# Performance work log

Measured on AMD Instinct MI355X. Metric: run time of the kernel, lower is better.

Reference implementation:

```python
import jax, jax.numpy as jnp
import numpy as np
import math

FMAPS = [(80, 0.06), (40, 0.12), (20, 0.24), (10, 0.48), (5, 0.72)]
SPLITS = [0, 6400, 8000, 8400, 8500, 8525]
N_LEVELS = 5
N_CAND = 9
ALPHA_REG = 1.0   # config.reg_weights
GAMMA, F_ALPHA = 2.0, 0.25


def _make_priors():
    ps = []
    for f, s in FMAPS:
        c = (np.arange(f, dtype=np.float32) + 0.5) / f
        cy, cx = np.meshgrid(c, c, indexing="ij")
        ps.append(np.stack([cx.ravel(), cy.ravel(),
                            np.full(f * f, s, np.float32),
                            np.full(f * f, s, np.float32)], 1))
    return jnp.asarray(np.concatenate(ps, 0))


def cxcy_to_xy(b):
    return jnp.concatenate([b[..., :2] - b[..., 2:] / 2, b[..., :2] + b[..., 2:] / 2], -1)


def xy_to_cxcy(b):
    return jnp.concatenate([(b[..., :2] + b[..., 2:]) / 2, b[..., 2:] - b[..., :2]], -1)


def gcxgcy_to_cxcy(g, priors):
    cxcy = g[..., :2] * priors[..., 2:] / 10.0 + priors[..., :2]
    wh = jnp.exp(g[..., 2:] / 5.0) * priors[..., 2:]
    return jnp.concatenate([cxcy, wh], -1)


def iou_matrix(a, b):  # a [K,4] corners, b [P,4] corners -> [K,P]
    lt = jnp.maximum(a[:, None, :2], b[None, :, :2])
    rb = jnp.minimum(a[:, None, 2:], b[None, :, 2:])
    wh = jnp.clip(rb - lt, 0.0)
    inter = wh[..., 0] * wh[..., 1]
    area_a = (a[:, 2] - a[:, 0]) * (a[:, 3] - a[:, 1])
    area_b = (b[:, 2] - b[:, 0]) * (b[:, 3] - b[:, 1])
    return inter / (area_a[:, None] + area_b[None, :] - inter)


def _assign_image(boxes_i, labels_i, locs_i, priors):
    # boxes_i [K,4] xyxy, labels_i [K] int, locs_i [P,4] encoded offsets
    gt_cxcy = xy_to_cxcy(boxes_i)
    per_level, pos_ov_all = [], []
    for l in range(N_LEVELS):
        pl = priors[SPLITS[l]:SPLITS[l + 1]]                       # [Pl,4] cxcywh
        dist = jnp.linalg.norm(gt_cxcy[:, None, :2] - pl[None, :, :2], axis=-1)  # [K,Pl]
        _, top_idx = jax.lax.top_k(-dist, N_CAND)                  # [K,9] closest priors
        ov = iou_matrix(boxes_i, cxcy_to_xy(pl))                   # [K,Pl]
        pos_ov = jnp.take_along_axis(ov, top_idx, axis=1)          # [K,9]
        pos_ov_all.append(pos_ov)
        per_level.append((pl, top_idx, pos_ov, locs_i[SPLITS[l]:SPLITS[l + 1]]))
    cat = jnp.concatenate(pos_ov_all, 1)                           # [K, 5*9]
    thr = cat.mean(1) + jnp.std(cat, axis=1, ddof=1)               # torch.std is unbiased

    labels_out, gt_match, dec_match, valid_all = [], [], [], []
    for l, (pl, top_idx, pos_ov, locs_l) in enumerate(per_level):
        cand = pl[top_idx]                                          # [K,9,4]
        inside = ((boxes_i[:, None, 0] < cand[..., 0]) & (cand[..., 0] < boxes_i[:, None, 2]) &
                  (boxes_i[:, None, 1] < cand[..., 1]) & (cand[..., 1] < boxes_i[:, None, 3]))
        cand_pos = (pos_ov > thr[:, None]) & inside                 # [K,9]
        masked = jnp.where(cand_pos, pos_ov, 0.0)                   # loop init current_max_iou=0
        best_ob = jnp.argmax(masked, axis=0)                        # [9], first-max == strict-> loop
        best_iou = jnp.max(masked, axis=0)
        valid = best_iou > 0.0                                      # [9]
        lab = jnp.where(valid, labels_i[best_ob], 0)
        Pl = SPLITS[l + 1] - SPLITS[l]
        # NB: original code indexes label array by candidate index c (bug kept faithfully)
        labels_out.append(jnp.zeros(Pl, jnp.int32).at[jnp.arange(N_CAND)].set(lab))
        decoded = cxcy_to_xy(gcxgcy_to_cxcy(locs_l, pl))            # [Pl,4]
        prior_idx = top_idx[best_ob, jnp.arange(N_CAND)]            # [9]
        dec_match.append(decoded[prior_idx])
        gt_match.append(boxes_i[best_ob])
        valid_all.append(valid)
    return (jnp.concatenate(labels_out),                            # [P]
            jnp.concatenate(gt_match, 0),                           # [45,4]
            jnp.concatenate(dec_match, 0),                          # [45,4]
            jnp.concatenate(valid_all))                             # [45]


def _ciou(pred, gt):  # corner boxes [N,4]
    w1, h1 = pred[:, 2] - pred[:, 0], pred[:, 3] - pred[:, 1]
    w2, h2 = gt[:, 2] - gt[:, 0], gt[:, 3] - gt[:, 1]
    lt = jnp.maximum(pred[:, :2], gt[:, :2]); rb = jnp.minimum(pred[:, 2:], gt[:, 2:])
    wh = jnp.clip(rb - lt, 0.0)
    inter = wh[:, 0] * wh[:, 1]
    union = w1 * h1 + w2 * h2 - inter
    iou = inter / union
    c1 = (pred[:, :2] + pred[:, 2:]) / 2; c2 = (gt[:, :2] + gt[:, 2:]) / 2
    rho2 = jnp.sum((c1 - c2) ** 2, -1)
    clt = jnp.minimum(pred[:, :2], gt[:, :2]); crb = jnp.maximum(pred[:, 2:], gt[:, 2:])
    cdiag = jnp.sum((crb - clt) ** 2, -1)
    v = (4.0 / math.pi ** 2) * (jnp.arctan(w2 / h2) - jnp.arctan(w1 / h1)) ** 2
    alpha = jax.lax.stop_gradient(v / (1.0 - iou + v))
    return jnp.clip(iou - rho2 / cdiag - alpha * v, -1.0, 1.0)


def _focal(logits, targets):  # logits [N,C], targets [N] in {0..C}, 0=background
    C = logits.shape[-1]
    cls = jnp.arange(1, C + 1)
    t = targets[:, None]
    p = jax.nn.sigmoid(logits)
    term1 = (1.0 - p) ** GAMMA * jax.nn.log_sigmoid(logits)
    term2 = p ** GAMMA * jax.nn.log_sigmoid(-logits)
    pos = (t == cls).astype(logits.dtype)
    neg = ((t != cls) & (t >= 0)).astype(logits.dtype)
    return -jnp.sum(pos * F_ALPHA * term1 + neg * (1.0 - F_ALPHA) * term2)


def setup_inputs():
    key = jax.random.key(0)
    k1, k2, k3, k4, k5 = jax.random.split(key, 5)
    B, K, C, P = 32, 16, 80, 8525
    lo = jax.random.uniform(k1, (B, K, 2), minval=0.05, maxval=0.55)
    sz = jax.random.uniform(k2, (B, K, 2), minval=0.08, maxval=0.35)
    boxes = jnp.concatenate([lo, lo + sz], -1)
    labels = jax.random.randint(k3, (B, K), 1, C + 1, dtype=jnp.int32)
    predicted_locs = jax.random.normal(k4, (B, P, 4), jnp.float32)
    predicted_scores = jax.random.normal(k5, (B, P, C), jnp.float32)
    return {"predicted_locs": predicted_locs, "predicted_scores": predicted_scores,
            "boxes": boxes, "labels": labels, "priors_cxcy": _make_priors()}


def reference(predicted_locs, predicted_scores, boxes, labels, priors_cxcy):
    tc, gt_m, dec_m, valid = jax.vmap(_assign_image, in_axes=(0, 0, 0, None))(
        boxes, labels, predicted_locs, priors_cxcy)
    tc_flat = tc.reshape(-1)
    n_pos = jnp.sum(tc_flat > 0).astype(jnp.float32)
    conf_loss = _focal(predicted_scores.reshape(-1, predicted_scores.shape[-1]), tc_flat) / n_pos
    ci = _ciou(dec_m.reshape(-1, 4), gt_m.reshape(-1, 4))
    vm = valid.reshape(-1).astype(jnp.float32)
    loc_loss = jnp.sum((1.0 - ci) * vm) / jnp.maximum(vm.sum(), 1.0)
    return conf_loss + ALPHA_REG * loc_loss
```

## Files before the change

### kernel.cpp

```cpp
#include <hip/hip_runtime.h>
#include <math.h>

#define KGT   16
#define NCAND 9
#define NLVL  5
#define NPRI  8525
#define NCLS  80
#define NIMG  32

#define SCAN_BLOCKS  10
#define FOCAL_BLOCKS 2038
#define TOTAL_BLOCKS 2048
#define NELEM (NIMG * NPRI * NCLS)
#define N4    (NELEM / 4)
#define NTASK (NIMG * KGT * NLVL)

#define OFF_IDXS  92160
#define OFF_PART  184320
#define OFF_IMG   192512

__device__ __forceinline__ float focal_elem(float x)
{
    float e  = __expf(-fabsf(x));
    float t  = 1.f + e;
    float r  = __builtin_amdgcn_rcpf(t);
    float sp = fmaxf(x, 0.f) + __logf(t);
    float nm = (x >= 0.f) ? 1.f : e;
    float p  = nm * r;
    return p * p * sp;
}

__device__ __forceinline__ float focal4(float4 v)
{
    return focal_elem(v.x) + focal_elem(v.y) + focal_elem(v.z) + focal_elem(v.w);
}

__global__ __launch_bounds__(256)
void atss_main(const float* __restrict__ scores,
               const float* __restrict__ boxes,
               const float* __restrict__ priors,
               float* __restrict__ povs,
               int*   __restrict__ idxs,
               float* __restrict__ partials)
{
    const int tid = threadIdx.x;
    const int blk = blockIdx.x;
    __shared__ float wsum[4];

    if (blk < SCAN_BLOCKS) {
        const int SPLc[5]  = {0, 6400, 8000, 8400, 8500};
        const int FDIM[5]  = {80, 40, 20, 10, 5};
        const int t = blk * 256 + tid;
        const int b = t / (KGT * NLVL);
        const int r = t % (KGT * NLVL);
        const int g = r / NLVL;
        const int l = r % NLVL;
        const int f    = FDIM[l];
        const int base = SPLc[l];

        float4 bx = ((const float4*)boxes)[b * KGT + g];
        const float gcx = (bx.x + bx.z) * 0.5f;
        const float gcy = (bx.y + bx.w) * 0.5f;

        const float ff = (float)f;
        int ix0 = (int)floorf(gcx * ff); ix0 = min(max(ix0, 0), f - 1);
        int iy0 = (int)floorf(gcy * ff); iy0 = min(max(iy0, 0), f - 1);
        int sx = min(max(ix0 - 2, 0), f - 5);
        int sy = min(max(iy0 - 2, 0), f - 5);

        unsigned long long L[NCAND];
        #pragma unroll
        for (int s = 0; s < NCAND; ++s) L[s] = ~0ull;

        for (int dy = 0; dy < 5; ++dy) {
            for (int dx = 0; dx < 5; ++dx) {
                int idx = (sy + dy) * f + (sx + dx);
                float2 pc = ((const float2*)priors)[(base + idx) * 2];
                float ddx = gcx - pc.x, ddy = gcy - pc.y;
                float dist = sqrtf(ddx * ddx + ddy * ddy);
                unsigned long long pk =
                    ((unsigned long long)__float_as_uint(dist) << 32) | (unsigned)idx;
                if (pk < L[NCAND - 1]) {
                    L[NCAND - 1] = pk;
                    #pragma unroll
                    for (int s = NCAND - 1; s >= 1; --s) {
                        if (L[s] < L[s - 1]) {
                            unsigned long long tw = L[s]; L[s] = L[s - 1]; L[s - 1] = tw;
                        } else break;
                    }
                }
            }
        }
        #pragma unroll
        for (int s = 0; s < NCAND; ++s) {
            int idx = (int)(unsigned)(L[s] & 0xffffffffull);
            float4 pr = ((const float4*)priors)[base + idx];
            float px0 = pr.x - pr.z * 0.5f, py0 = pr.y - pr.w * 0.5f;
            float px1 = pr.x + pr.z * 0.5f, py1 = pr.y + pr.w * 0.5f;
            float iw = fmaxf(fminf(bx.z, px1) - fmaxf(bx.x, px0), 0.f);
            float ih = fmaxf(fminf(bx.w, py1) - fmaxf(bx.y, py0), 0.f);
            float inter = iw * ih;
            float areaA = (bx.z - bx.x) * (bx.w - bx.y);
            float areaP = (px1 - px0) * (py1 - py0);
            povs[t * NCAND + s] = inter / (areaA + areaP - inter);
            idxs[t * NCAND + s] = idx;
        }
        return;
    }

    const float4* s4 = (const float4*)scores;
    const int S = FOCAL_BLOCKS * 256;
    int gid = (blk - SCAN_BLOCKS) * 256 + tid;
    float lsum = 0.f;
    for (int bse = gid; bse < N4; bse += 4 * S) {
        int i1 = bse + S, i2 = bse + 2 * S, i3 = bse + 3 * S;
        float4 v0 = s4[bse];
        float4 v1 = s4[min(i1, N4 - 1)];
        float4 v2 = s4[min(i2, N4 - 1)];
        float4 v3 = s4[min(i3, N4 - 1)];
        float t0 = focal4(v0);
        float t1 = focal4(v1);
        float t2 = focal4(v2);
        float t3 = focal4(v3);
        lsum += t0;
        lsum += (i1 < N4) ? t1 : 0.f;
        lsum += (i2 < N4) ? t2 : 0.f;
        lsum += (i3 < N4) ? t3 : 0.f;
    }
    #pragma unroll
    for (int off = 32; off > 0; off >>= 1) lsum += __shfl_down(lsum, off);
    if ((tid & 63) == 0) wsum[tid >> 6] = lsum;
    __syncthreads();
    if (tid == 0)
        partials[blk - SCAN_BLOCKS] = wsum[0] + wsum[1] + wsum[2] + wsum[3];
}

__global__ __launch_bounds__(256)
void atss_decide(const float* __restrict__ locs,
                 const float* __restrict__ scores,
                 const float* __restrict__ boxes,
                 const int*   __restrict__ labels,
                 const float* __restrict__ priors,
                 const float* __restrict__ povs,
                 const int*   __restrict__ idxs,
                 float* __restrict__ imgstats)
{
    const int tid = threadIdx.x;
    const int b = blockIdx.x;
    const int SPLc[6] = {0, 6400, 8000, 8400, 8500, 8525};

    __shared__ float pov[KGT * 45];
    __shared__ int   tix[KGT * 45];
    __shared__ float sbox[KGT][4];
    __shared__ int   slab[KGT];
    __shared__ float thr[KGT];
    __shared__ float rc, rl;
    __shared__ int   rn;

    if (tid == 0) { rc = 0.f; rl = 0.f; rn = 0; }
    for (int e = tid; e < KGT * 45; e += 256) {
        pov[e] = povs[b * (KGT * 45) + e];
        tix[e] = idxs[b * (KGT * 45) + e];
    }
    if (tid < KGT) {
        float4 bxv = ((const float4*)boxes)[b * KGT + tid];
        sbox[tid][0] = bxv.x; sbox[tid][1] = bxv.y;
        sbox[tid][2] = bxv.z; sbox[tid][3] = bxv.w;
        slab[tid] = labels[b * KGT + tid];
    }
    __syncthreads();

    if (tid < KGT) {
        float s = 0.f;
        for (int q = 0; q < 45; ++q) s += pov[tid * 45 + q];
        float mean = s / 45.f;
        float ss = 0.f;
        for (int q = 0; q < 45; ++q) { float d = pov[tid * 45 + q] - mean; ss += d * d; }
        thr[tid] = mean + sqrtf(ss / 44.f);
    }
    __syncthreads();

    if (tid < NLVL * NCAND) {
        int l = tid / NCAND, j = tid % NCAND;
        float bestv = -1.f; int bestg = 0;
        #pragma unroll
        for (int gg = 0; gg < KGT; ++gg) {
            float m = pov[gg * 45 + tid];
            int pi = tix[gg * 45 + tid];
            float4 pr = ((const float4*)priors)[SPLc[l] + pi];
            bool inside = (sbox[gg][0] < pr.x) && (pr.x < sbox[gg][2]) &&
                          (sbox[gg][1] < pr.y) && (pr.y < sbox[gg][3]);
            float mm = ((m > thr[gg]) && inside) ? m : 0.f;
            if (mm > bestv) { bestv = mm; bestg = gg; }
        }
        if (bestv > 0.f) {
            int lab = slab[bestg];
            long pos = (long)b * NPRI + SPLc[l] + j;
            float x  = scores[pos * NCLS + (lab - 1)];
            float e  = expf(-fabsf(x));
            float l1 = log1pf(e);
            float spp = fmaxf(x, 0.f) + l1;
            float spn = fmaxf(-x, 0.f) + l1;
            float p   = (x >= 0.f) ? 1.f / (1.f + e) : e / (1.f + e);
            float corr = 0.25f * (1.f - p) * (1.f - p) * spn - 0.75f * p * p * spp;

            int pi = tix[bestg * 45 + tid];
            float4 pr = ((const float4*)priors)[SPLc[l] + pi];
            float4 lc = ((const float4*)locs)[b * NPRI + SPLc[l] + pi];
            float cx = lc.x * pr.z / 10.f + pr.x;
            float cy = lc.y * pr.w / 10.f + pr.y;
            float w  = expf(lc.z / 5.f) * pr.z;
            float h  = expf(lc.w / 5.f) * pr.w;
            float qx0 = cx - w * 0.5f, qy0 = cy - h * 0.5f;
            float qx1 = cx + w * 0.5f, qy1 = cy + h * 0.5f;
            float gx0 = sbox[bestg][0], gy0 = sbox[bestg][1];
            float gx1 = sbox[bestg][2], gy1 = sbox[bestg][3];
            float w1 = qx1 - qx0, h1 = qy1 - qy0, w2 = gx1 - gx0, h2 = gy1 - gy0;
            float iw = fmaxf(fminf(qx1, gx1) - fmaxf(qx0, gx0), 0.f);
            float ih = fmaxf(fminf(qy1, gy1) - fmaxf(qy0, gy0), 0.f);
            float inter = iw * ih;
            float iou = inter / (w1 * h1 + w2 * h2 - inter);
            float dcx = (qx0 + qx1) * 0.5f - (gx0 + gx1) * 0.5f;
            float dcy = (qy0 + qy1) * 0.5f - (gy0 + gy1) * 0.5f;
            float rho2 = dcx * dcx + dcy * dcy;
            float ex = fmaxf(qx1, gx1) - fminf(qx0, gx0);
            float ey = fmaxf(qy1, gy1) - fminf(qy0, gy0);
            float cdiag = ex * ex + ey * ey;
            float da = atanf(w2 / h2) - atanf(w1 / h1);
            float v  = 0.4052847345693511f * da * da;
            float alpha = v / (1.f - iou + v);
            float ci = iou - rho2 / cdiag - alpha * v;
            ci = fminf(fmaxf(ci, -1.f), 1.f);

            atomicAdd(&rc, corr);
            atomicAdd(&rl, 1.f - ci);
            atomicAdd(&rn, 1);
        }
    }
    __syncthreads();
    if (tid == 0) {
        imgstats[b * 3 + 0] = rc;
        imgstats[b * 3 + 1] = rl;
        imgstats[b * 3 + 2] = (float)rn;
    }
}

__global__ __launch_bounds__(256)
void atss_finalize(const float* __restrict__ partials,
                   const float* __restrict__ imgstats,
                   float* __restrict__ out)
{
    const int tid = threadIdx.x;
    __shared__ float wsum[4];
    float lsum = 0.f;
    for (int i = tid; i < FOCAL_BLOCKS; i += 256) lsum += partials[i];
    #pragma unroll
    for (int off = 32; off > 0; off >>= 1) lsum += __shfl_down(lsum, off);
    if ((tid & 63) == 0) wsum[tid >> 6] = lsum;
    __syncthreads();
    if (tid == 0) {
        float base = 0.75f * (wsum[0] + wsum[1] + wsum[2] + wsum[3]);
        float corr = 0.f, loc = 0.f, cnt = 0.f;
        for (int b = 0; b < NIMG; ++b) {
            corr += imgstats[b * 3 + 0];
            loc  += imgstats[b * 3 + 1];
            cnt  += imgstats[b * 3 + 2];
        }
        float conf = (base + corr) / cnt;
        float locl = loc / fmaxf(cnt, 1.f);
        out[0] = conf + locl;
    }
}

extern "C" void kernel_launch(void* const* d_in, const int* in_sizes, int n_in,
                              void* d_out, int out_size, void* d_ws, size_t ws_size,
                              hipStream_t stream)
{
    const float* locs   = (const float*)d_in[0];
    const float* scores = (const float*)d_in[1];
    const float* boxes  = (const float*)d_in[2];
    const int*   labels = (const int*)d_in[3];
    const float* priors = (const float*)d_in[4];
    float* out = (float*)d_out;

    float* povs     = (float*)d_ws;
    int*   idxs     = (int*)((char*)d_ws + OFF_IDXS);
    float* partials = (float*)((char*)d_ws + OFF_PART);
    float* imgstats = (float*)((char*)d_ws + OFF_IMG);

    atss_main<<<TOTAL_BLOCKS, 256, 0, stream>>>(scores, boxes, priors,
                                                povs, idxs, partials);
    atss_decide<<<NIMG, 256, 0, stream>>>(locs, scores, boxes, labels, priors,
                                          povs, idxs, imgstats);
    atss_finalize<<<1, 256, 0, stream>>>(partials, imgstats, out);
}
```

Measured before the change: 155.3 us.

## Fuse per-image ATSS assignment into focal-loss kernel, dropping the decide launch

```diff
diff --git a/kernel.cpp b/kernel.cpp
--- a/kernel.cpp
+++ b/kernel.cpp
@@ -8,16 +8,12 @@
 #define NCLS  80
 #define NIMG  32
 
-#define SCAN_BLOCKS  10
-#define FOCAL_BLOCKS 2038
-#define TOTAL_BLOCKS 2048
+#define FOCAL_BLOCKS 2016
+#define TOTAL_BLOCKS (NIMG + FOCAL_BLOCKS)
 #define NELEM (NIMG * NPRI * NCLS)
 #define N4    (NELEM / 4)
-#define NTASK (NIMG * KGT * NLVL)
-
-#define OFF_IDXS  92160
-#define OFF_PART  184320
-#define OFF_IMG   192512
+
+#define OFF_IMG 8064
 
 __device__ __forceinline__ float focal_elem(float x)
 {
@@ -36,81 +32,180 @@
 }
 
 __global__ __launch_bounds__(256)
-void atss_main(const float* __restrict__ scores,
-               const float* __restrict__ boxes,
-               const float* __restrict__ priors,
-               float* __restrict__ povs,
-               int*   __restrict__ idxs,
-               float* __restrict__ partials)
+void atss_fused(const float* __restrict__ locs,
+                const float* __restrict__ scores,
+                const float* __restrict__ boxes,
+                const int*   __restrict__ labels,
+                const float* __restrict__ priors,
+                float* __restrict__ partials,
+                float* __restrict__ imgstats)
 {
     const int tid = threadIdx.x;
     const int blk = blockIdx.x;
+
+    __shared__ float pov[KGT * 45];
+    __shared__ int   tix[KGT * 45];
+    __shared__ float sbox[KGT][4];
+    __shared__ int   slab[KGT];
+    __shared__ float thr[KGT];
+    __shared__ float rc, rl;
+    __shared__ int   rn;
     __shared__ float wsum[4];
 
-    if (blk < SCAN_BLOCKS) {
-        const int SPLc[5]  = {0, 6400, 8000, 8400, 8500};
-        const int FDIM[5]  = {80, 40, 20, 10, 5};
-        const int t = blk * 256 + tid;
-        const int b = t / (KGT * NLVL);
-        const int r = t % (KGT * NLVL);
-        const int g = r / NLVL;
-        const int l = r % NLVL;
-        const int f    = FDIM[l];
-        const int base = SPLc[l];
-
-        float4 bx = ((const float4*)boxes)[b * KGT + g];
-        const float gcx = (bx.x + bx.z) * 0.5f;
-        const float gcy = (bx.y + bx.w) * 0.5f;
-
-        const float ff = (float)f;
-        int ix0 = (int)floorf(gcx * ff); ix0 = min(max(ix0, 0), f - 1);
-        int iy0 = (int)floorf(gcy * ff); iy0 = min(max(iy0, 0), f - 1);
-        int sx = min(max(ix0 - 2, 0), f - 5);
-        int sy = min(max(iy0 - 2, 0), f - 5);
-
-        unsigned long long L[NCAND];
-        #pragma unroll
-        for (int s = 0; s < NCAND; ++s) L[s] = ~0ull;
-
-        for (int dy = 0; dy < 5; ++dy) {
-            for (int dx = 0; dx < 5; ++dx) {
-                int idx = (sy + dy) * f + (sx + dx);
-                float2 pc = ((const float2*)priors)[(base + idx) * 2];
-                float ddx = gcx - pc.x, ddy = gcy - pc.y;
-                float dist = sqrtf(ddx * ddx + ddy * ddy);
-                unsigned long long pk =
-                    ((unsigned long long)__float_as_uint(dist) << 32) | (unsigned)idx;
-                if (pk < L[NCAND - 1]) {
-                    L[NCAND - 1] = pk;
-                    #pragma unroll
-                    for (int s = NCAND - 1; s >= 1; --s) {
-                        if (L[s] < L[s - 1]) {
-                            unsigned long long tw = L[s]; L[s] = L[s - 1]; L[s - 1] = tw;
-                        } else break;
+    if (blk < NIMG) {
+        const int b = blk;
+        const int SPLc[6] = {0, 6400, 8000, 8400, 8500, 8525};
+        const int FDIM[5] = {80, 40, 20, 10, 5};
+
+        if (tid == 0) { rc = 0.f; rl = 0.f; rn = 0; }
+        if (tid < KGT) {
+            float4 bxv = ((const float4*)boxes)[b * KGT + tid];
+            sbox[tid][0] = bxv.x; sbox[tid][1] = bxv.y;
+            sbox[tid][2] = bxv.z; sbox[tid][3] = bxv.w;
+            slab[tid] = labels[b * KGT + tid];
+        }
+
+        if (tid < KGT * NLVL) {
+            const int g    = tid / NLVL;
+            const int l    = tid % NLVL;
+            const int f    = FDIM[l];
+            const int base = SPLc[l];
+
+            float4 bx = ((const float4*)boxes)[b * KGT + g];
+            const float gcx = (bx.x + bx.z) * 0.5f;
+            const float gcy = (bx.y + bx.w) * 0.5f;
+
+            const float ff = (float)f;
+            int ix0 = (int)floorf(gcx * ff); ix0 = min(max(ix0, 0), f - 1);
+            int iy0 = (int)floorf(gcy * ff); iy0 = min(max(iy0, 0), f - 1);
+            int sx = min(max(ix0 - 2, 0), f - 5);
+            int sy = min(max(iy0 - 2, 0), f - 5);
+
+            unsigned long long L[NCAND];
+            #pragma unroll
+            for (int s = 0; s < NCAND; ++s) L[s] = ~0ull;
+
+            for (int dy = 0; dy < 5; ++dy) {
+                for (int dx = 0; dx < 5; ++dx) {
+                    int idx = (sy + dy) * f + (sx + dx);
+                    float2 pc = ((const float2*)priors)[(base + idx) * 2];
+                    float ddx = gcx - pc.x, ddy = gcy - pc.y;
+                    float dist = sqrtf(ddx * ddx + ddy * ddy);
+                    unsigned long long pk =
+                        ((unsigned long long)__float_as_uint(dist) << 32) |
+                        (unsigned)idx;
+                    if (pk < L[NCAND - 1]) {
+                        L[NCAND - 1] = pk;
+                        #pragma unroll
+                        for (int s = NCAND - 1; s >= 1; --s) {
+                            if (L[s] < L[s - 1]) {
+                                unsigned long long tw = L[s];
+                                L[s] = L[s - 1]; L[s - 1] = tw;
+                            } else break;
+                        }
                     }
                 }
             }
-        }
-        #pragma unroll
-        for (int s = 0; s < NCAND; ++s) {
-            int idx = (int)(unsigned)(L[s] & 0xffffffffull);
-            float4 pr = ((const float4*)priors)[base + idx];
-            float px0 = pr.x - pr.z * 0.5f, py0 = pr.y - pr.w * 0.5f;
-            float px1 = pr.x + pr.z * 0.5f, py1 = pr.y + pr.w * 0.5f;
-            float iw = fmaxf(fminf(bx.z, px1) - fmaxf(bx.x, px0), 0.f);
-            float ih = fmaxf(fminf(bx.w, py1) - fmaxf(bx.y, py0), 0.f);
-            float inter = iw * ih;
-            float areaA = (bx.z - bx.x) * (bx.w - bx.y);
-            float areaP = (px1 - px0) * (py1 - py0);
-            povs[t * NCAND + s] = inter / (areaA + areaP - inter);
-            idxs[t * NCAND + s] = idx;
+            #pragma unroll
+            for (int s = 0; s < NCAND; ++s) {
+                int idx = (int)(unsigned)(L[s] & 0xffffffffull);
+                float4 pr = ((const float4*)priors)[base + idx];
+                float px0 = pr.x - pr.z * 0.5f, py0 = pr.y - pr.w * 0.5f;
+                float px1 = pr.x + pr.z * 0.5f, py1 = pr.y + pr.w * 0.5f;
+                float iw = fmaxf(fminf(bx.z, px1) - fmaxf(bx.x, px0), 0.f);
+                float ih = fmaxf(fminf(bx.w, py1) - fmaxf(bx.y, py0), 0.f);
+                float inter = iw * ih;
+                float areaA = (bx.z - bx.x) * (bx.w - bx.y);
+                float areaP = (px1 - px0) * (py1 - py0);
+                pov[tid * NCAND + s] = inter / (areaA + areaP - inter);
+                tix[tid * NCAND + s] = idx;
+            }
+        }
+        __syncthreads();
+
+        if (tid < KGT) {
+            float s = 0.f;
+            for (int q = 0; q < 45; ++q) s += pov[tid * 45 + q];
+            float mean = s / 45.f;
+            float ss = 0.f;
+            for (int q = 0; q < 45; ++q) {
+                float d = pov[tid * 45 + q] - mean; ss += d * d;
+            }
+            thr[tid] = mean + sqrtf(ss / 44.f);
+        }
+        __syncthreads();
+
+        if (tid < NLVL * NCAND) {
+            int l = tid / NCAND, j = tid % NCAND;
+            float bestv = -1.f; int bestg = 0;
+            #pragma unroll
+            for (int gg = 0; gg < KGT; ++gg) {
+                float m = pov[gg * 45 + tid];
+                int pi = tix[gg * 45 + tid];
+                float4 pr = ((const float4*)priors)[SPLc[l] + pi];
+                bool inside = (sbox[gg][0] < pr.x) && (pr.x < sbox[gg][2]) &&
+                              (sbox[gg][1] < pr.y) && (pr.y < sbox[gg][3]);
+                float mm = ((m > thr[gg]) && inside) ? m : 0.f;
+                if (mm > bestv) { bestv = mm; bestg = gg; }
+            }
+            if (bestv > 0.f) {
+                int lab = slab[bestg];
+                long pos = (long)b * NPRI + SPLc[l] + j;
+                float x  = scores[pos * NCLS + (lab - 1)];
+                float e  = expf(-fabsf(x));
+                float l1 = log1pf(e);
+                float spp = fmaxf(x, 0.f) + l1;
+                float spn = fmaxf(-x, 0.f) + l1;
+                float p   = (x >= 0.f) ? 1.f / (1.f + e) : e / (1.f + e);
+                float corr = 0.25f * (1.f - p) * (1.f - p) * spn
+                           - 0.75f * p * p * spp;
+
+                int pi = tix[bestg * 45 + tid];
+                float4 pr = ((const float4*)priors)[SPLc[l] + pi];
+                float4 lc = ((const float4*)locs)[b * NPRI + SPLc[l] + pi];
+                float cx = lc.x * pr.z / 10.f + pr.x;
+                float cy = lc.y * pr.w / 10.f + pr.y;
+                float w  = expf(lc.z / 5.f) * pr.z;
+                float h  = expf(lc.w / 5.f) * pr.w;
+                float qx0 = cx - w * 0.5f, qy0 = cy - h * 0.5f;
+                float qx1 = cx + w * 0.5f, qy1 = cy + h * 0.5f;
+                float gx0 = sbox[bestg][0], gy0 = sbox[bestg][1];
+                float gx1 = sbox[bestg][2], gy1 = sbox[bestg][3];
+                float w1 = qx1 - qx0, h1 = qy1 - qy0;
+                float w2 = gx1 - gx0, h2 = gy1 - gy0;
+                float iw = fmaxf(fminf(qx1, gx1) - fmaxf(qx0, gx0), 0.f);
+                float ih = fmaxf(fminf(qy1, gy1) - fmaxf(qy0, gy0), 0.f);
+                float inter = iw * ih;
+                float iou = inter / (w1 * h1 + w2 * h2 - inter);
+                float dcx = (qx0 + qx1) * 0.5f - (gx0 + gx1) * 0.5f;
+                float dcy = (qy0 + qy1) * 0.5f - (gy0 + gy1) * 0.5f;
+                float rho2 = dcx * dcx + dcy * dcy;
+                float ex = fmaxf(qx1, gx1) - fminf(qx0, gx0);
+                float ey = fmaxf(qy1, gy1) - fminf(qy0, gy0);
+                float cdiag = ex * ex + ey * ey;
+                float da = atanf(w2 / h2) - atanf(w1 / h1);
+                float v  = 0.4052847345693511f * da * da;
+                float alpha = v / (1.f - iou + v);
+                float ci = iou - rho2 / cdiag - alpha * v;
+                ci = fminf(fmaxf(ci, -1.f), 1.f);
+
+                atomicAdd(&rc, corr);
+                atomicAdd(&rl, 1.f - ci);
+                atomicAdd(&rn, 1);
+            }
+        }
+        __syncthreads();
+        if (tid == 0) {
+            imgstats[b * 3 + 0] = rc;
+            imgstats[b * 3 + 1] = rl;
+            imgstats[b * 3 + 2] = (float)rn;
         }
         return;
     }
 
     const float4* s4 = (const float4*)scores;
     const int S = FOCAL_BLOCKS * 256;
-    int gid = (blk - SCAN_BLOCKS) * 256 + tid;
+    int gid = (blk - NIMG) * 256 + tid;
     float lsum = 0.f;
     for (int bse = gid; bse < N4; bse += 4 * S) {
         int i1 = bse + S, i2 = bse + 2 * S, i3 = bse + 3 * S;
@@ -132,117 +227,7 @@
     if ((tid & 63) == 0) wsum[tid >> 6] = lsum;
     __syncthreads();
     if (tid == 0)
-        partials[blk - SCAN_BLOCKS] = wsum[0] + wsum[1] + wsum[2] + wsum[3];
-}
-
-__global__ __launch_bounds__(256)
-void atss_decide(const float* __restrict__ locs,
-                 const float* __restrict__ scores,
-                 const float* __restrict__ boxes,
-                 const int*   __restrict__ labels,
-                 const float* __restrict__ priors,
-                 const float* __restrict__ povs,
-                 const int*   __restrict__ idxs,
-                 float* __restrict__ imgstats)
-{
-    const int tid = threadIdx.x;
-    const int b = blockIdx.x;
-    const int SPLc[6] = {0, 6400, 8000, 8400, 8500, 8525};
-
-    __shared__ float pov[KGT * 45];
-    __shared__ int   tix[KGT * 45];
-    __shared__ float sbox[KGT][4];
-    __shared__ int   slab[KGT];
-    __shared__ float thr[KGT];
-    __shared__ float rc, rl;
-    __shared__ int   rn;
-
-    if (tid == 0) { rc = 0.f; rl = 0.f; rn = 0; }
-    for (int e = tid; e < KGT * 45; e += 256) {
-        pov[e] = povs[b * (KGT * 45) + e];
-        tix[e] = idxs[b * (KGT * 45) + e];
-    }
-    if (tid < KGT) {
-        float4 bxv = ((const float4*)boxes)[b * KGT + tid];
-        sbox[tid][0] = bxv.x; sbox[tid][1] = bxv.y;
-        sbox[tid][2] = bxv.z; sbox[tid][3] = bxv.w;
-        slab[tid] = labels[b * KGT + tid];
-    }
-    __syncthreads();
-
-    if (tid < KGT) {
-        float s = 0.f;
-        for (int q = 0; q < 45; ++q) s += pov[tid * 45 + q];
-        float mean = s / 45.f;
-        float ss = 0.f;
-        for (int q = 0; q < 45; ++q) { float d = pov[tid * 45 + q] - mean; ss += d * d; }
-        thr[tid] = mean + sqrtf(ss / 44.f);
-    }
-    __syncthreads();
-
-    if (tid < NLVL * NCAND) {
-        int l = tid / NCAND, j = tid % NCAND;
-        float bestv = -1.f; int bestg = 0;
-        #pragma unroll
-        for (int gg = 0; gg < KGT; ++gg) {
-            float m = pov[gg * 45 + tid];
-            int pi = tix[gg * 45 + tid];
-            float4 pr = ((const float4*)priors)[SPLc[l] + pi];
-            bool inside = (sbox[gg][0] < pr.x) && (pr.x < sbox[gg][2]) &&
-                          (sbox[gg][1] < pr.y) && (pr.y < sbox[gg][3]);
-            float mm = ((m > thr[gg]) && inside) ? m : 0.f;
-            if (mm > bestv) { bestv = mm; bestg = gg; }
-        }
-        if (bestv > 0.f) {
-            int lab = slab[bestg];
-            long pos = (long)b * NPRI + SPLc[l] + j;
-            float x  = scores[pos * NCLS + (lab - 1)];
-            float e  = expf(-fabsf(x));
-            float l1 = log1pf(e);
-            float spp = fmaxf(x, 0.f) + l1;
-            float spn = fmaxf(-x, 0.f) + l1;
-            float p   = (x >= 0.f) ? 1.f / (1.f + e) : e / (1.f + e);
-            float corr = 0.25f * (1.f - p) * (1.f - p) * spn - 0.75f * p * p * spp;
-
-            int pi = tix[bestg * 45 + tid];
-            float4 pr = ((const float4*)priors)[SPLc[l] + pi];
-            float4 lc = ((const float4*)locs)[b * NPRI + SPLc[l] + pi];
-            float cx = lc.x * pr.z / 10.f + pr.x;
-            float cy = lc.y * pr.w / 10.f + pr.y;
-            float w  = expf(lc.z / 5.f) * pr.z;
-            float h  = expf(lc.w / 5.f) * pr.w;
-            float qx0 = cx - w * 0.5f, qy0 = cy - h * 0.5f;
-            float qx1 = cx + w * 0.5f, qy1 = cy + h * 0.5f;
-            float gx0 = sbox[bestg][0], gy0 = sbox[bestg][1];
-            float gx1 = sbox[bestg][2], gy1 = sbox[bestg][3];
-            float w1 = qx1 - qx0, h1 = qy1 - qy0, w2 = gx1 - gx0, h2 = gy1 - gy0;
-            float iw = fmaxf(fminf(qx1, gx1) - fmaxf(qx0, gx0), 0.f);
-            float ih = fmaxf(fminf(qy1, gy1) - fmaxf(qy0, gy0), 0.f);
-            float inter = iw * ih;
-            float iou = inter / (w1 * h1 + w2 * h2 - inter);
-            float dcx = (qx0 + qx1) * 0.5f - (gx0 + gx1) * 0.5f;
-            float dcy = (qy0 + qy1) * 0.5f - (gy0 + gy1) * 0.5f;
-            float rho2 = dcx * dcx + dcy * dcy;
-            float ex = fmaxf(qx1, gx1) - fminf(qx0, gx0);
-            float ey = fmaxf(qy1, gy1) - fminf(qy0, gy0);
-            float cdiag = ex * ex + ey * ey;
-            float da = atanf(w2 / h2) - atanf(w1 / h1);
-            float v  = 0.4052847345693511f * da * da;
-            float alpha = v / (1.f - iou + v);
-            float ci = iou - rho2 / cdiag - alpha * v;
-            ci = fminf(fmaxf(ci, -1.f), 1.f);
-
-            atomicAdd(&rc, corr);
-            atomicAdd(&rl, 1.f - ci);
-            atomicAdd(&rn, 1);
-        }
-    }
-    __syncthreads();
-    if (tid == 0) {
-        imgstats[b * 3 + 0] = rc;
-        imgstats[b * 3 + 1] = rl;
-        imgstats[b * 3 + 2] = (float)rn;
-    }
+        partials[blk - NIMG] = wsum[0] + wsum[1] + wsum[2] + wsum[3];
 }
 
 __global__ __launch_bounds__(256)
@@ -283,14 +268,10 @@
     const float* priors = (const float*)d_in[4];
     float* out = (float*)d_out;
 
-    float* povs     = (float*)d_ws;
-    int*   idxs     = (int*)((char*)d_ws + OFF_IDXS);
-    float* partials = (float*)((char*)d_ws + OFF_PART);
+    float* partials = (float*)d_ws;
     float* imgstats = (float*)((char*)d_ws + OFF_IMG);
 
-    atss_main<<<TOTAL_BLOCKS, 256, 0, stream>>>(scores, boxes, priors,
-                                                povs, idxs, partials);
-    atss_decide<<<NIMG, 256, 0, stream>>>(locs, scores, boxes, labels, priors,
-                                          povs, idxs, imgstats);
+    atss_fused<<<TOTAL_BLOCKS, 256, 0, stream>>>(locs, scores, boxes, labels,
+                                                 priors, partials, imgstats);
     atss_finalize<<<1, 256, 0, stream>>>(partials, imgstats, out);
 }
```

Measured after the change: 151.8 us. 1.02x faster.
